# Kernel optimization log

Measured on AMD Instinct MI355X. Metric: run time of the kernel, lower is better.

Reference implementation:

```python
import jax, jax.numpy as jnp
import numpy as np

D_MODEL = 256
N_HEADS = 8
N_LEVELS = 4
N_POINTS = 4
DH = D_MODEL // N_HEADS
SHAPES = [(100, 150), (50, 75), (25, 38), (13, 19)]  # per-level (H, W)
BATCH = 2


def setup_inputs() -> dict:
    key = jax.random.key(0)
    ks = jax.random.split(key, 8)
    Lq = sum(h * w for h, w in SHAPES)  # 19947
    d = D_MODEL
    off_dim = N_HEADS * N_LEVELS * N_POINTS * 2
    aw_dim = N_HEADS * N_LEVELS * N_POINTS
    s = 1.0 / np.sqrt(d).astype(np.float32)
    lsi = np.concatenate([[0], np.cumsum([h * w for h, w in SHAPES])[:-1]])
    return {
        "query": jax.random.normal(ks[0], (BATCH, Lq, d), jnp.float32),
        "reference_points": jax.random.uniform(ks[1], (BATCH, Lq, N_LEVELS, 2), jnp.float32),
        "input_flatten": jax.random.normal(ks[2], (BATCH, Lq, d), jnp.float32),
        "input_spatial_shapes": jnp.array(SHAPES, dtype=jnp.int32),
        "input_level_start_index": jnp.array(lsi, dtype=jnp.int32),
        "W_samp": 0.01 * jax.random.normal(ks[3], (off_dim, d), jnp.float32),
        "b_samp": 0.1 * jax.random.normal(ks[4], (off_dim,), jnp.float32),
        "W_attn": s * jax.random.normal(ks[5], (aw_dim, d), jnp.float32),
        "b_attn": jnp.zeros((aw_dim,), jnp.float32),
        "W_val": s * jax.random.normal(ks[6], (d, d), jnp.float32),
        "b_val": jnp.zeros((d,), jnp.float32),
        "W_out": s * jax.random.normal(ks[7], (d, d), jnp.float32),
        "b_out": jnp.zeros((d,), jnp.float32),
    }


def _bilinear(v, grid, Hl, Wl):
    # v: [N, H, Hl*Wl, Dh] flattened level feature map per head
    # grid: [N, H, Q, P, 2] in [-1, 1]; align_corners=False, zero padding
    N, H, Q, P, _ = grid.shape
    Dh = v.shape[-1]
    x = (grid[..., 0] + 1.0) * 0.5 * Wl - 0.5
    y = (grid[..., 1] + 1.0) * 0.5 * Hl - 0.5
    x0 = jnp.floor(x)
    y0 = jnp.floor(y)
    lx = x - x0
    ly = y - y0
    x0i = x0.astype(jnp.int32)
    y0i = y0.astype(jnp.int32)

    def corner(xi, yi, w):
        valid = (xi >= 0) & (xi < Wl) & (yi >= 0) & (yi < Hl)
        idx = jnp.clip(yi, 0, Hl - 1) * Wl + jnp.clip(xi, 0, Wl - 1)
        g = jnp.take_along_axis(v, idx.reshape(N, H, Q * P, 1), axis=2)
        return g.reshape(N, H, Q, P, Dh) * (w * valid)[..., None]

    return (corner(x0i, y0i, (1 - lx) * (1 - ly))
            + corner(x0i + 1, y0i, lx * (1 - ly))
            + corner(x0i, y0i + 1, (1 - lx) * ly)
            + corner(x0i + 1, y0i + 1, lx * ly))


def _forward(query, ref, x, shapes, W_samp, b_samp, W_attn, b_attn, W_val, b_val, W_out, b_out):
    N, Lq, d = query.shape
    H, L, P, Dh = N_HEADS, N_LEVELS, N_POINTS, DH
    # value projection -> [N, H, S, Dh]
    value = (x @ W_val.T + b_val).reshape(N, -1, H, Dh).transpose(0, 2, 1, 3)
    off = (query @ W_samp.T + b_samp).reshape(N, Lq, H, L, P, 2)
    attw = jax.nn.softmax((query @ W_attn.T + b_attn).reshape(N, Lq, H, L * P), axis=-1)
    attw = attw.reshape(N, Lq, H, L, P).transpose(0, 2, 1, 3, 4)  # [N,H,Lq,L,P]
    # offset normalizer is (W, H) per level
    norm = jnp.array([[w, h] for h, w in shapes], dtype=query.dtype)  # [L, 2]
    loc = ref[:, :, None, :, None, :] + off / norm[None, None, None, :, None, :]
    grids = (2.0 * loc - 1.0).transpose(0, 2, 1, 3, 4, 5)  # [N,H,Lq,L,P,2]

    acc = jnp.zeros((N, Lq, H, Dh), query.dtype)
    start = 0
    for lvl, (Hl, Wl) in enumerate(shapes):
        v = value[:, :, start:start + Hl * Wl]  # [N,H,Hl*Wl,Dh]
        start += Hl * Wl
        samp = _bilinear(v, grids[:, :, :, lvl], Hl, Wl)  # [N,H,Lq,P,Dh]
        acc = acc + jnp.einsum('nhqpd,nhqp->nqhd', samp, attw[:, :, :, lvl])
    out = acc.reshape(N, Lq, H * Dh)
    return out @ W_out.T + b_out


def reference(query, reference_points, input_flatten, input_spatial_shapes,
              input_level_start_index, W_samp, b_samp, W_attn, b_attn,
              W_val, b_val, W_out, b_out):
    shapes = [(int(h), int(w)) for h, w in np.asarray(input_spatial_shapes)]
    return _forward(query, reference_points, input_flatten, shapes,
                    W_samp, b_samp, W_attn, b_attn, W_val, b_val, W_out, b_out)
```

## Files before the change

kernel.cpp:

```cpp
#include <hip/hip_runtime.h>
#include <hip/hip_bf16.h>

#define NB 2
#define LQ 19947
#define LV 19947
#define DM 256
#define NH 8
#define NL 4
#define NP 4
#define MROWS (NB*LQ)
#define MPAD  39936
#define QPB 2

__device__ __constant__ int c_lvlH[4] = {100, 50, 25, 13};
__device__ __constant__ int c_lvlW[4] = {150, 75, 38, 19};
__device__ __constant__ int c_lvlS[4] = {0, 15000, 18750, 19700};

typedef __attribute__((ext_vector_type(8))) short short8;
typedef __attribute__((ext_vector_type(4))) float f32x4;
typedef __attribute__((ext_vector_type(2))) float f32x2;

__device__ __forceinline__ unsigned short f2bf(float f) {
  unsigned u = __float_as_uint(f);
  u += 0x7FFFu + ((u >> 16) & 1u);
  return (unsigned short)(u >> 16);
}
__device__ __forceinline__ float bfl(unsigned u) { return __uint_as_float(u << 16); }
__device__ __forceinline__ float bfh(unsigned u) { return __uint_as_float(u & 0xFFFF0000u); }
__device__ __forceinline__ f32x2 up2(unsigned u) {
  f32x2 r; r.x = __uint_as_float(u << 16); r.y = __uint_as_float(u & 0xFFFF0000u); return r;
}

#define CB_X 9984
__global__ __launch_bounds__(256) void conv_all(
    const float* __restrict__ xin, const float* __restrict__ query,
    const float* __restrict__ Wv, const float* __restrict__ Wsamp,
    const float* __restrict__ Wattn, const float* __restrict__ Wout,
    const float* __restrict__ bsamp, const float* __restrict__ battn,
    unsigned short* __restrict__ xb, unsigned short* __restrict__ qb,
    unsigned short* __restrict__ wvb, unsigned short* __restrict__ wqb,
    unsigned short* __restrict__ wob, float* __restrict__ bsa)
{
  const int b = blockIdx.x, t = threadIdx.x;
  if (b == 2 * CB_X + 224) {
    bsa[t] = bsamp[t];
    if (t < 128) bsa[256 + t] = battn[t];
    return;
  }
  const float* src; unsigned short* dst; int base, ns;
  if (b < CB_X)            { src = xin;   dst = xb;          base = b * 1024;                ns = MROWS * 256; }
  else if (b < 2*CB_X)     { src = query; dst = qb;          base = (b - CB_X) * 1024;       ns = MROWS * 256; }
  else if (b < 2*CB_X+64)  { src = Wv;    dst = wvb;         base = (b - 2*CB_X) * 1024;     ns = 65536; }
  else if (b < 2*CB_X+128) { src = Wsamp; dst = wqb;         base = (b - 2*CB_X-64) * 1024;  ns = 65536; }
  else if (b < 2*CB_X+160) { src = Wattn; dst = wqb + 65536; base = (b - 2*CB_X-128) * 1024; ns = 32768; }
  else                     { src = Wout;  dst = wob;         base = (b - 2*CB_X-160) * 1024; ns = 65536; }
  const int i = base + t * 4;
  ushort4 o;
  if (i + 4 <= ns) {
    const float4 v = *(const float4*)(src + i);
    o.x = f2bf(v.x); o.y = f2bf(v.y); o.z = f2bf(v.z); o.w = f2bf(v.w);
  } else {
    float vs[4];
    #pragma unroll
    for (int j = 0; j < 4; ++j) vs[j] = (i + j < ns) ? src[i + j] : 0.f;
    o.x = f2bf(vs[0]); o.y = f2bf(vs[1]); o.z = f2bf(vs[2]); o.w = f2bf(vs[3]);
  }
  *(ushort4*)(dst + i) = o;
}

__global__ __launch_bounds__(256) void gemm_front(
    const unsigned short* __restrict__ xb, const unsigned short* __restrict__ qb,
    const unsigned short* __restrict__ wvb, const unsigned short* __restrict__ wqb,
    const float* __restrict__ b_val, const float* __restrict__ bsa,
    unsigned short* __restrict__ value, unsigned short* __restrict__ oc)
{
  const unsigned short* Ab; const unsigned short* Wb; const float* bias;
  unsigned short* Cp; int Nn, cb;
  if (blockIdx.y < 2) { Ab = xb; Wb = wvb; bias = b_val; Cp = value; Nn = 256; cb = blockIdx.y; }
  else                { Ab = qb; Wb = wqb; bias = bsa;   Cp = oc;    Nn = 384; cb = blockIdx.y - 2; }

  __shared__ alignas(16) short As[128 * 32];
  __shared__ alignas(16) short Bs[128 * 32];

  const int t = threadIdx.x;
  const int w = t >> 6, l = t & 63;
  const int wr = w >> 1, wc = w & 1;
  const size_t rowBase = (size_t)blockIdx.x * 128;
  const int colBase = cb * 128;

  const f32x4 z = {0.f, 0.f, 0.f, 0.f};
  f32x4 acc[4][4];
  #pragma unroll
  for (int i = 0; i < 4; ++i)
    #pragma unroll
    for (int j = 0; j < 4; ++j) acc[i][j] = z;

  const int srow = l >> 2;
  const int scol = (l & 3) * 8;

  for (int ks = 0; ks < 8; ++ks) {
    const int k0 = ks * 32;
    #pragma unroll
    for (int i = 0; i < 2; ++i) {
      const int ii = w * 2 + i;
      const unsigned short* gA = Ab + (rowBase + ii * 16 + srow) * 256 + k0 + scol;
      __builtin_amdgcn_global_load_lds(
          (const __attribute__((address_space(1))) void*)gA,
          (__attribute__((address_space(3))) void*)&As[ii * 512], 16, 0, 0);
      const unsigned short* gB = Wb + ((size_t)(colBase + ii * 16 + srow)) * 256 + k0 + scol;
      __builtin_amdgcn_global_load_lds(
          (const __attribute__((address_space(1))) void*)gB,
          (__attribute__((address_space(3))) void*)&Bs[ii * 512], 16, 0, 0);
    }
    __syncthreads();
    short8 af[4], bf[4];
    #pragma unroll
    for (int i = 0; i < 4; ++i) {
      af[i] = *(const short8*)&As[(wr * 64 + i * 16 + (l & 15)) * 32 + (l >> 4) * 8];
      bf[i] = *(const short8*)&Bs[(wc * 64 + i * 16 + (l & 15)) * 32 + (l >> 4) * 8];
    }
    #pragma unroll
    for (int i = 0; i < 4; ++i)
      #pragma unroll
      for (int j = 0; j < 4; ++j)
        acc[i][j] = __builtin_amdgcn_mfma_f32_16x16x32_bf16(bf[j], af[i], acc[i][j], 0, 0, 0);
    __syncthreads();
  }

  const int row0 = (int)rowBase + wr * 64 + (l & 15);
  const int col0 = colBase + wc * 64 + (l >> 4) * 4;
  #pragma unroll
  for (int j = 0; j < 4; ++j) {
    const float4 bj = *(const float4*)(bias + col0 + j * 16);
    #pragma unroll
    for (int i = 0; i < 4; ++i) {
      const int row = row0 + i * 16;
      uint2 st;
      st.x = (unsigned)f2bf(acc[i][j][0] + bj.x) | ((unsigned)f2bf(acc[i][j][1] + bj.y) << 16);
      st.y = (unsigned)f2bf(acc[i][j][2] + bj.z) | ((unsigned)f2bf(acc[i][j][3] + bj.w) << 16);
      *(uint2*)(Cp + (size_t)row * Nn + col0 + j * 16) = st;
    }
  }
}

__global__ __launch_bounds__(256) void gemm_out(
    const unsigned short* __restrict__ Ab, const unsigned short* __restrict__ Wb,
    const float* __restrict__ bias, float* __restrict__ Cp)
{
  __shared__ alignas(16) short As[128 * 32];
  __shared__ alignas(16) short Bs[128 * 32];

  const int t = threadIdx.x;
  const int w = t >> 6, l = t & 63;
  const int wr = w >> 1, wc = w & 1;
  const size_t rowBase = (size_t)blockIdx.x * 128;
  const int colBase = blockIdx.y * 128;

  const f32x4 z = {0.f, 0.f, 0.f, 0.f};
  f32x4 acc[4][4];
  #pragma unroll
  for (int i = 0; i < 4; ++i)
    #pragma unroll
    for (int j = 0; j < 4; ++j) acc[i][j] = z;

  const int srow = l >> 2;
  const int scol = (l & 3) * 8;

  for (int ks = 0; ks < 8; ++ks) {
    const int k0 = ks * 32;
    #pragma unroll
    for (int i = 0; i < 2; ++i) {
      const int ii = w * 2 + i;
      const unsigned short* gA = Ab + (rowBase + ii * 16 + srow) * 256 + k0 + scol;
      __builtin_amdgcn_global_load_lds(
          (const __attribute__((address_space(1))) void*)gA,
          (__attribute__((address_space(3))) void*)&As[ii * 512], 16, 0, 0);
      const unsigned short* gB = Wb + ((size_t)(colBase + ii * 16 + srow)) * 256 + k0 + scol;
      __builtin_amdgcn_global_load_lds(
          (const __attribute__((address_space(1))) void*)gB,
          (__attribute__((address_space(3))) void*)&Bs[ii * 512], 16, 0, 0);
    }
    __syncthreads();
    short8 af[4], bf[4];
    #pragma unroll
    for (int i = 0; i < 4; ++i) {
      af[i] = *(const short8*)&As[(wr * 64 + i * 16 + (l & 15)) * 32 + (l >> 4) * 8];
      bf[i] = *(const short8*)&Bs[(wc * 64 + i * 16 + (l & 15)) * 32 + (l >> 4) * 8];
    }
    #pragma unroll
    for (int i = 0; i < 4; ++i)
      #pragma unroll
      for (int j = 0; j < 4; ++j)
        acc[i][j] = __builtin_amdgcn_mfma_f32_16x16x32_bf16(bf[j], af[i], acc[i][j], 0, 0, 0);
    __syncthreads();
  }

  const int row0 = (int)rowBase + wr * 64 + (l & 15);
  const int col0 = colBase + wc * 64 + (l >> 4) * 4;
  #pragma unroll
  for (int j = 0; j < 4; ++j) {
    const float4 bj = *(const float4*)(bias + col0 + j * 16);
    #pragma unroll
    for (int i = 0; i < 4; ++i) {
      const int row = row0 + i * 16;
      if (row < MROWS) {
        *(float4*)(Cp + (size_t)row * 256 + col0 + j * 16) =
            make_float4(acc[i][j][0] + bj.x, acc[i][j][1] + bj.y,
                        acc[i][j][2] + bj.z, acc[i][j][3] + bj.w);
      }
    }
  }
}

__global__ __launch_bounds__(128) void msda_sample(
    const unsigned short* __restrict__ value,
    const float* __restrict__ refp,
    const unsigned short* __restrict__ oc,
    unsigned short* __restrict__ accb)
{
  __shared__ float s_aw[QPB][128];
  __shared__ float s_ref[QPB][8];
  __shared__ alignas(16) unsigned s_pk[QPB][NH][17][8];

  const int t = threadIdx.x;
  const int bq0 = blockIdx.x * QPB;

  {
    const int q = t >> 6, i = t & 63;
    const int bq = bq0 + q;
    const unsigned pw = *(const unsigned*)(oc + (size_t)bq * 384 + 256 + i * 2);
    s_aw[q][i * 2 + 0] = bfl(pw);
    s_aw[q][i * 2 + 1] = bfh(pw);
    if (t < QPB * 8) {
      const int q2 = t >> 3, j = t & 7;
      s_ref[q2][j] = refp[(size_t)(bq0 + q2) * 8 + j];
    }
  }
  __syncthreads();

  if (t < QPB * NH) {
    const int q = t >> 3, h = t & 7;
    float* aw = &s_aw[q][h * 16];
    float m = aw[0];
    #pragma unroll
    for (int i = 1; i < 16; ++i) m = fmaxf(m, aw[i]);
    float e[16]; float s = 0.f;
    #pragma unroll
    for (int i = 0; i < 16; ++i) { e[i] = __expf(aw[i] - m); s += e[i]; }
    const float inv = 1.f / s;
    #pragma unroll
    for (int i = 0; i < 16; ++i) aw[i] = e[i] * inv;
  }
  __syncthreads();

  #pragma unroll
  for (int it = t; it < QPB * 128; it += 128) {
    const int q = it >> 7, rem = it & 127;
    const int h = rem >> 4, idx = rem & 15;
    const int l = idx >> 2;
    const int bq = bq0 + q;
    const unsigned po = *(const unsigned*)(oc + (size_t)bq * 384 + rem * 2);
    const int Hl = c_lvlH[l], Wl = c_lvlW[l], st = c_lvlS[l];
    const float x = s_ref[q][l * 2 + 0] * (float)Wl - 0.5f + bfl(po);
    const float y = s_ref[q][l * 2 + 1] * (float)Hl - 0.5f + bfh(po);
    const float aw = s_aw[q][rem];
    const float x0f = floorf(x), y0f = floorf(y);
    const float lx = x - x0f, ly = y - y0f;
    const int x0 = (int)x0f, y0 = (int)y0f;
    const float vx0 = (x0 >= 0 && x0 < Wl) ? 1.f : 0.f;
    const float vx1 = (x0 >= -1 && x0 < Wl - 1) ? 1.f : 0.f;
    const float vy0 = (y0 >= 0 && y0 < Hl) ? 1.f : 0.f;
    const float vy1 = (y0 >= -1 && y0 < Hl - 1) ? 1.f : 0.f;
    const int xc0 = min(max(x0, 0), Wl - 1);
    const int xc1 = min(max(x0 + 1, 0), Wl - 1);
    const int yc0 = min(max(y0, 0), Hl - 1);
    const int yc1 = min(max(y0 + 1, 0), Hl - 1);
    const int r0 = st + yc0 * Wl, r1 = st + yc1 * Wl;
    uint4 g0, g1;
    g0.x = (unsigned)(r0 + xc0) * 512u;
    g0.y = (unsigned)(r0 + xc1) * 512u;
    g0.z = __float_as_uint((1.f - lx) * (1.f - ly) * aw * (vx0 * vy0));
    g0.w = __float_as_uint(lx * (1.f - ly) * aw * (vx1 * vy0));
    g1.x = (unsigned)(r1 + xc0) * 512u;
    g1.y = (unsigned)(r1 + xc1) * 512u;
    g1.z = __float_as_uint((1.f - lx) * ly * aw * (vx0 * vy1));
    g1.w = __float_as_uint(lx * ly * aw * (vx1 * vy1));
    *(uint4*)&s_pk[q][h][idx][0] = g0;
    *(uint4*)&s_pk[q][h][idx][4] = g1;
  }
  __syncthreads();

  const int wv = t >> 6;
  const int lane = t & 63;
  const int bq = bq0 + wv;
  const int n = bq / LQ;
  const char* vbase = (const char*)value + (size_t)n * LV * 512;
  const int h = lane >> 3;
  const int c2 = (lane >> 2) & 1;
  const unsigned laneoff = (unsigned)(h * 64 + (lane & 3) * 16);

  f32x2 acc0 = {0.f, 0.f}, acc1 = {0.f, 0.f}, acc2 = {0.f, 0.f}, acc3 = {0.f, 0.f};

#define PKRD(i) (*(const uint4*)&s_pk[wv][h][(i)][c2 * 4])
#define GLD(o)  (*(const uint4*)(vbase + (o) + laneoff))

  uint4 pk0 = PKRD(0), pk1 = PKRD(1), pk2 = PKRD(2), pk3 = PKRD(3);
  uint4 va0 = GLD(pk0.x), vb0 = GLD(pk0.y);
  uint4 va1 = GLD(pk1.x), vb1 = GLD(pk1.y);
  uint4 va2 = GLD(pk2.x), vb2 = GLD(pk2.y);

  #pragma unroll
  for (int idx = 0; idx < 16; ++idx) {
    uint4 va3, vb3, pk4;
    if (idx < 13) { va3 = GLD(pk3.x); vb3 = GLD(pk3.y); }
    if (idx < 12) { pk4 = PKRD(idx + 4); }
    const float was = __uint_as_float(pk0.z);
    const float wbs = __uint_as_float(pk0.w);
    f32x2 wa; wa.x = was; wa.y = was;
    f32x2 wb; wb.x = wbs; wb.y = wbs;
    acc0 = acc0 + wa * up2(va0.x);
    acc1 = acc1 + wa * up2(va0.y);
    acc2 = acc2 + wa * up2(va0.z);
    acc3 = acc3 + wa * up2(va0.w);
    acc0 = acc0 + wb * up2(vb0.x);
    acc1 = acc1 + wb * up2(vb0.y);
    acc2 = acc2 + wb * up2(vb0.z);
    acc3 = acc3 + wb * up2(vb0.w);
    pk0 = pk1; pk1 = pk2; pk2 = pk3; pk3 = pk4;
    va0 = va1; va1 = va2; va2 = va3;
    vb0 = vb1; vb1 = vb2; vb2 = vb3;
  }
#undef PKRD
#undef GLD

  acc0.x += __shfl_xor(acc0.x, 4); acc0.y += __shfl_xor(acc0.y, 4);
  acc1.x += __shfl_xor(acc1.x, 4); acc1.y += __shfl_xor(acc1.y, 4);
  acc2.x += __shfl_xor(acc2.x, 4); acc2.y += __shfl_xor(acc2.y, 4);
  acc3.x += __shfl_xor(acc3.x, 4); acc3.y += __shfl_xor(acc3.y, 4);

  if (c2 == 0) {
    uint4 st;
    st.x = (unsigned)f2bf(acc0.x) | ((unsigned)f2bf(acc0.y) << 16);
    st.y = (unsigned)f2bf(acc1.x) | ((unsigned)f2bf(acc1.y) << 16);
    st.z = (unsigned)f2bf(acc2.x) | ((unsigned)f2bf(acc2.y) << 16);
    st.w = (unsigned)f2bf(acc3.x) | ((unsigned)f2bf(acc3.y) << 16);
    *(uint4*)((char*)accb + (size_t)bq * 512 + laneoff) = st;
  }
}

extern "C" void kernel_launch(void* const* d_in, const int* in_sizes, int n_in,
                              void* d_out, int out_size, void* d_ws, size_t ws_size,
                              hipStream_t stream) {
  const float* query  = (const float*)d_in[0];
  const float* refp   = (const float*)d_in[1];
  const float* xin    = (const float*)d_in[2];
  const float* W_samp = (const float*)d_in[5];
  const float* b_samp = (const float*)d_in[6];
  const float* W_attn = (const float*)d_in[7];
  const float* b_attn = (const float*)d_in[8];
  const float* W_val  = (const float*)d_in[9];
  const float* b_val  = (const float*)d_in[10];
  const float* W_out  = (const float*)d_in[11];
  const float* b_out  = (const float*)d_in[12];
  float* out = (float*)d_out;
  (void)in_sizes; (void)n_in; (void)out_size; (void)ws_size;

  char* ws = (char*)d_ws;
  unsigned short* value = (unsigned short*)(ws);
  unsigned short* qb    = (unsigned short*)(ws + 20447232);
  unsigned short* xb    = (unsigned short*)(ws + 40894464);
  unsigned short* accb  = xb;
  unsigned short* oc    = (unsigned short*)(ws + 61341696);
  unsigned short* wvb   = (unsigned short*)(ws + 92012544);
  unsigned short* wqb   = (unsigned short*)(ws + 92143616);
  unsigned short* wob   = (unsigned short*)(ws + 92340224);
  float*          bsa   = (float*)(ws + 92471296);

  hipLaunchKernelGGL(conv_all, dim3(2 * CB_X + 225), dim3(256), 0, stream,
                     xin, query, W_val, W_samp, W_attn, W_out, b_samp, b_attn,
                     xb, qb, wvb, wqb, wob, bsa);
  hipLaunchKernelGGL(gemm_front, dim3(312, 5), dim3(256), 0, stream,
                     xb, qb, wvb, wqb, b_val, bsa, value, oc);
  hipLaunchKernelGGL(msda_sample, dim3(MROWS / QPB), dim3(128), 0, stream,
                     value, refp, oc, accb);
  hipLaunchKernelGGL(gemm_out, dim3(312, 2), dim3(256), 0, stream,
                     accb, wob, b_out, out);
}
```

Before: 247.0 us.

## Fuse fp32-to-bf16 conversion into GEMM tile loads and drop conversion kernel

Removes the separate conv_all kernel that converted the inputs and weights to bf16 in workspace. The GEMMs now load fp32 tiles straight from global memory, convert them in registers with v_cvt_pk_bf16_f32 and write them to an XOR-swizzled LDS layout. The next tile is prefetched into registers while the MFMAs run. This saves a kernel launch and a full write-then-reread of the bf16 copies, at the cost of fp32 global reads of twice the width inside the GEMM. The weights are also re-converted by every block.

```diff
diff --git a/kernel.cpp b/kernel.cpp
--- a/kernel.cpp
+++ b/kernel.cpp
@@ -30,54 +30,30 @@
 __device__ __forceinline__ f32x2 up2(unsigned u) {
   f32x2 r; r.x = __uint_as_float(u << 16); r.y = __uint_as_float(u & 0xFFFF0000u); return r;
 }
-
-#define CB_X 9984
-__global__ __launch_bounds__(256) void conv_all(
+__device__ __forceinline__ unsigned cvtpk(float lo, float hi) {
+  unsigned r;
+  asm("v_cvt_pk_bf16_f32 %0, %1, %2" : "=v"(r) : "v"(lo), "v"(hi));
+  return r;
+}
+
+__global__ __launch_bounds__(256) void gemm_front(
     const float* __restrict__ xin, const float* __restrict__ query,
     const float* __restrict__ Wv, const float* __restrict__ Wsamp,
-    const float* __restrict__ Wattn, const float* __restrict__ Wout,
-    const float* __restrict__ bsamp, const float* __restrict__ battn,
-    unsigned short* __restrict__ xb, unsigned short* __restrict__ qb,
-    unsigned short* __restrict__ wvb, unsigned short* __restrict__ wqb,
-    unsigned short* __restrict__ wob, float* __restrict__ bsa)
-{
-  const int b = blockIdx.x, t = threadIdx.x;
-  if (b == 2 * CB_X + 224) {
-    bsa[t] = bsamp[t];
-    if (t < 128) bsa[256 + t] = battn[t];
-    return;
-  }
-  const float* src; unsigned short* dst; int base, ns;
-  if (b < CB_X)            { src = xin;   dst = xb;          base = b * 1024;                ns = MROWS * 256; }
-  else if (b < 2*CB_X)     { src = query; dst = qb;          base = (b - CB_X) * 1024;       ns = MROWS * 256; }
-  else if (b < 2*CB_X+64)  { src = Wv;    dst = wvb;         base = (b - 2*CB_X) * 1024;     ns = 65536; }
-  else if (b < 2*CB_X+128) { src = Wsamp; dst = wqb;         base = (b - 2*CB_X-64) * 1024;  ns = 65536; }
-  else if (b < 2*CB_X+160) { src = Wattn; dst = wqb + 65536; base = (b - 2*CB_X-128) * 1024; ns = 32768; }
-  else                     { src = Wout;  dst = wob;         base = (b - 2*CB_X-160) * 1024; ns = 65536; }
-  const int i = base + t * 4;
-  ushort4 o;
-  if (i + 4 <= ns) {
-    const float4 v = *(const float4*)(src + i);
-    o.x = f2bf(v.x); o.y = f2bf(v.y); o.z = f2bf(v.z); o.w = f2bf(v.w);
-  } else {
-    float vs[4];
-    #pragma unroll
-    for (int j = 0; j < 4; ++j) vs[j] = (i + j < ns) ? src[i + j] : 0.f;
-    o.x = f2bf(vs[0]); o.y = f2bf(vs[1]); o.z = f2bf(vs[2]); o.w = f2bf(vs[3]);
-  }
-  *(ushort4*)(dst + i) = o;
-}
-
-__global__ __launch_bounds__(256) void gemm_front(
-    const unsigned short* __restrict__ xb, const unsigned short* __restrict__ qb,
-    const unsigned short* __restrict__ wvb, const unsigned short* __restrict__ wqb,
-    const float* __restrict__ b_val, const float* __restrict__ bsa,
+    const float* __restrict__ Wattn,
+    const float* __restrict__ b_val, const float* __restrict__ b_samp,
+    const float* __restrict__ b_attn,
     unsigned short* __restrict__ value, unsigned short* __restrict__ oc)
 {
-  const unsigned short* Ab; const unsigned short* Wb; const float* bias;
-  unsigned short* Cp; int Nn, cb;
-  if (blockIdx.y < 2) { Ab = xb; Wb = wvb; bias = b_val; Cp = value; Nn = 256; cb = blockIdx.y; }
-  else                { Ab = qb; Wb = wqb; bias = bsa;   Cp = oc;    Nn = 384; cb = blockIdx.y - 2; }
+  const float* Af; const float* Bf; const float* biasp;
+  unsigned short* Cp; int Nn, cb, bro;
+  if (blockIdx.y < 2) {
+    Af = xin; Bf = Wv; cb = blockIdx.y; bro = cb * 128;
+    biasp = b_val + cb * 128; Cp = value; Nn = 256;
+  } else {
+    Af = query; cb = blockIdx.y - 2; Cp = oc; Nn = 384;
+    if (cb < 2) { Bf = Wsamp; bro = cb * 128; biasp = b_samp + cb * 128; }
+    else        { Bf = Wattn; bro = 0;        biasp = b_attn; }
+  }
 
   __shared__ alignas(16) short As[128 * 32];
   __shared__ alignas(16) short Bs[128 * 32];
@@ -95,43 +71,65 @@
     #pragma unroll
     for (int j = 0; j < 4; ++j) acc[i][j] = z;
 
-  const int srow = l >> 2;
-  const int scol = (l & 3) * 8;
+  const int srow = t >> 1;
+  const int skh  = (t & 1) * 16;
+  const int swzW = (srow & 2) << 2;
+  const int arow_ok = ((int)rowBase + srow) < MROWS;
+  const float* apBase = Af + ((size_t)rowBase + srow) * 256 + skh;
+  const float* bpBase = Bf + (size_t)(bro + srow) * 256 + skh;
+  short* pA0 = &As[((srow * 32 + skh) ^ swzW)];
+  short* pA1 = &As[((srow * 32 + skh + 8) ^ swzW)];
+  short* pB0 = &Bs[((srow * 32 + skh) ^ swzW)];
+  short* pB1 = &Bs[((srow * 32 + skh + 8) ^ swzW)];
+  const float4 fz4 = make_float4(0.f, 0.f, 0.f, 0.f);
+
+  float4 a0, a1, a2, a3, b0, b1, b2, b3;
+#define LOADA(K) do { if (arow_ok) { const float* ap = apBase + (K); \
+    a0 = *(const float4*)ap; a1 = *(const float4*)(ap + 4); \
+    a2 = *(const float4*)(ap + 8); a3 = *(const float4*)(ap + 12); } \
+    else { a0 = fz4; a1 = fz4; a2 = fz4; a3 = fz4; } } while (0)
+#define LOADB(K) do { const float* bp = bpBase + (K); \
+    b0 = *(const float4*)bp; b1 = *(const float4*)(bp + 4); \
+    b2 = *(const float4*)(bp + 8); b3 = *(const float4*)(bp + 12); } while (0)
+
+  LOADA(0); LOADB(0);
 
   for (int ks = 0; ks < 8; ++ks) {
-    const int k0 = ks * 32;
-    #pragma unroll
-    for (int i = 0; i < 2; ++i) {
-      const int ii = w * 2 + i;
-      const unsigned short* gA = Ab + (rowBase + ii * 16 + srow) * 256 + k0 + scol;
-      __builtin_amdgcn_global_load_lds(
-          (const __attribute__((address_space(1))) void*)gA,
-          (__attribute__((address_space(3))) void*)&As[ii * 512], 16, 0, 0);
-      const unsigned short* gB = Wb + ((size_t)(colBase + ii * 16 + srow)) * 256 + k0 + scol;
-      __builtin_amdgcn_global_load_lds(
-          (const __attribute__((address_space(1))) void*)gB,
-          (__attribute__((address_space(3))) void*)&Bs[ii * 512], 16, 0, 0);
-    }
     __syncthreads();
+    uint4 wA0, wA1, wB0, wB1;
+    wA0.x = cvtpk(a0.x, a0.y); wA0.y = cvtpk(a0.z, a0.w);
+    wA0.z = cvtpk(a1.x, a1.y); wA0.w = cvtpk(a1.z, a1.w);
+    wA1.x = cvtpk(a2.x, a2.y); wA1.y = cvtpk(a2.z, a2.w);
+    wA1.z = cvtpk(a3.x, a3.y); wA1.w = cvtpk(a3.z, a3.w);
+    wB0.x = cvtpk(b0.x, b0.y); wB0.y = cvtpk(b0.z, b0.w);
+    wB0.z = cvtpk(b1.x, b1.y); wB0.w = cvtpk(b1.z, b1.w);
+    wB1.x = cvtpk(b2.x, b2.y); wB1.y = cvtpk(b2.z, b2.w);
+    wB1.z = cvtpk(b3.x, b3.y); wB1.w = cvtpk(b3.z, b3.w);
+    *(uint4*)pA0 = wA0; *(uint4*)pA1 = wA1;
+    *(uint4*)pB0 = wB0; *(uint4*)pB1 = wB1;
+    __syncthreads();
+    if (ks < 7) { LOADA((ks + 1) * 32); LOADB((ks + 1) * 32); }
     short8 af[4], bf[4];
     #pragma unroll
     for (int i = 0; i < 4; ++i) {
-      af[i] = *(const short8*)&As[(wr * 64 + i * 16 + (l & 15)) * 32 + (l >> 4) * 8];
-      bf[i] = *(const short8*)&Bs[(wc * 64 + i * 16 + (l & 15)) * 32 + (l >> 4) * 8];
+      af[i] = *(const short8*)&As[(((wr * 64 + i * 16 + (l & 15)) * 32 + (l >> 4) * 8)) ^ ((l & 2) << 2)];
+      bf[i] = *(const short8*)&Bs[(((wc * 64 + i * 16 + (l & 15)) * 32 + (l >> 4) * 8)) ^ ((l & 2) << 2)];
     }
     #pragma unroll
     for (int i = 0; i < 4; ++i)
       #pragma unroll
       for (int j = 0; j < 4; ++j)
         acc[i][j] = __builtin_amdgcn_mfma_f32_16x16x32_bf16(bf[j], af[i], acc[i][j], 0, 0, 0);
-    __syncthreads();
-  }
+  }
+#undef LOADA
+#undef LOADB
 
   const int row0 = (int)rowBase + wr * 64 + (l & 15);
-  const int col0 = colBase + wc * 64 + (l >> 4) * 4;
+  const int lc0 = wc * 64 + (l >> 4) * 4;
+  const int col0 = colBase + lc0;
   #pragma unroll
   for (int j = 0; j < 4; ++j) {
-    const float4 bj = *(const float4*)(bias + col0 + j * 16);
+    const float4 bj = *(const float4*)(biasp + lc0 + j * 16);
     #pragma unroll
     for (int i = 0; i < 4; ++i) {
       const int row = row0 + i * 16;
@@ -144,7 +142,7 @@
 }
 
 __global__ __launch_bounds__(256) void gemm_out(
-    const unsigned short* __restrict__ Ab, const unsigned short* __restrict__ Wb,
+    const unsigned short* __restrict__ Ab, const float* __restrict__ Wof,
     const float* __restrict__ bias, float* __restrict__ Cp)
 {
   __shared__ alignas(16) short As[128 * 32];
@@ -163,37 +161,54 @@
     #pragma unroll
     for (int j = 0; j < 4; ++j) acc[i][j] = z;
 
-  const int srow = l >> 2;
-  const int scol = (l & 3) * 8;
+  const int lrow = l >> 2;
+  const int lcol = (l & 3) * 8;
+  const int srow = t >> 1;
+  const int skh  = (t & 1) * 16;
+  const int swzW = (srow & 2) << 2;
+  const float* bpBase = Wof + (size_t)(colBase + srow) * 256 + skh;
+  short* pB0 = &Bs[((srow * 32 + skh) ^ swzW)];
+  short* pB1 = &Bs[((srow * 32 + skh + 8) ^ swzW)];
+
+  float4 b0, b1, b2, b3;
+#define LOADB(K) do { const float* bp = bpBase + (K); \
+    b0 = *(const float4*)bp; b1 = *(const float4*)(bp + 4); \
+    b2 = *(const float4*)(bp + 8); b3 = *(const float4*)(bp + 12); } while (0)
+
+  LOADB(0);
 
   for (int ks = 0; ks < 8; ++ks) {
     const int k0 = ks * 32;
+    __syncthreads();
     #pragma unroll
     for (int i = 0; i < 2; ++i) {
       const int ii = w * 2 + i;
-      const unsigned short* gA = Ab + (rowBase + ii * 16 + srow) * 256 + k0 + scol;
+      const unsigned short* gA = Ab + (rowBase + ii * 16 + lrow) * 256 + k0 + lcol;
       __builtin_amdgcn_global_load_lds(
           (const __attribute__((address_space(1))) void*)gA,
           (__attribute__((address_space(3))) void*)&As[ii * 512], 16, 0, 0);
-      const unsigned short* gB = Wb + ((size_t)(colBase + ii * 16 + srow)) * 256 + k0 + scol;
-      __builtin_amdgcn_global_load_lds(
-          (const __attribute__((address_space(1))) void*)gB,
-          (__attribute__((address_space(3))) void*)&Bs[ii * 512], 16, 0, 0);
-    }
+    }
+    uint4 wB0, wB1;
+    wB0.x = cvtpk(b0.x, b0.y); wB0.y = cvtpk(b0.z, b0.w);
+    wB0.z = cvtpk(b1.x, b1.y); wB0.w = cvtpk(b1.z, b1.w);
+    wB1.x = cvtpk(b2.x, b2.y); wB1.y = cvtpk(b2.z, b2.w);
+    wB1.z = cvtpk(b3.x, b3.y); wB1.w = cvtpk(b3.z, b3.w);
+    *(uint4*)pB0 = wB0; *(uint4*)pB1 = wB1;
     __syncthreads();
+    if (ks < 7) LOADB((ks + 1) * 32);
     short8 af[4], bf[4];
     #pragma unroll
     for (int i = 0; i < 4; ++i) {
       af[i] = *(const short8*)&As[(wr * 64 + i * 16 + (l & 15)) * 32 + (l >> 4) * 8];
-      bf[i] = *(const short8*)&Bs[(wc * 64 + i * 16 + (l & 15)) * 32 + (l >> 4) * 8];
+      bf[i] = *(const short8*)&Bs[(((wc * 64 + i * 16 + (l & 15)) * 32 + (l >> 4) * 8)) ^ ((l & 2) << 2)];
     }
     #pragma unroll
     for (int i = 0; i < 4; ++i)
       #pragma unroll
       for (int j = 0; j < 4; ++j)
         acc[i][j] = __builtin_amdgcn_mfma_f32_16x16x32_bf16(bf[j], af[i], acc[i][j], 0, 0, 0);
-    __syncthreads();
-  }
+  }
+#undef LOADB
 
   const int row0 = (int)rowBase + wr * 64 + (l & 15);
   const int col0 = colBase + wc * 64 + (l >> 4) * 4;
@@ -367,22 +382,14 @@
 
   char* ws = (char*)d_ws;
   unsigned short* value = (unsigned short*)(ws);
-  unsigned short* qb    = (unsigned short*)(ws + 20447232);
-  unsigned short* xb    = (unsigned short*)(ws + 40894464);
-  unsigned short* accb  = xb;
-  unsigned short* oc    = (unsigned short*)(ws + 61341696);
-  unsigned short* wvb   = (unsigned short*)(ws + 92012544);
-  unsigned short* wqb   = (unsigned short*)(ws + 92143616);
-  unsigned short* wob   = (unsigned short*)(ws + 92340224);
-  float*          bsa   = (float*)(ws + 92471296);
-
-  hipLaunchKernelGGL(conv_all, dim3(2 * CB_X + 225), dim3(256), 0, stream,
-                     xin, query, W_val, W_samp, W_attn, W_out, b_samp, b_attn,
-                     xb, qb, wvb, wqb, wob, bsa);
+  unsigned short* accb  = (unsigned short*)(ws + 20447232);
+  unsigned short* oc    = (unsigned short*)(ws + 40894464);
+
   hipLaunchKernelGGL(gemm_front, dim3(312, 5), dim3(256), 0, stream,
-                     xb, qb, wvb, wqb, b_val, bsa, value, oc);
+                     xin, query, W_val, W_samp, W_attn, b_val, b_samp, b_attn,
+                     value, oc);
   hipLaunchKernelGGL(msda_sample, dim3(MROWS / QPB), dim3(128), 0, stream,
                      value, refp, oc, accb);
   hipLaunchKernelGGL(gemm_out, dim3(312, 2), dim3(256), 0, stream,
-                     accb, wob, b_out, out);
-}
+                     accb, W_out, b_out, out);
+}
```

After: 247.1 us. No clear change (+0.0%).
